# Optimization experiments

Hardware: AMD Instinct MI355X
Metric: run time of the kernel (lower is better)

Reference implementation:

```python
import jax, jax.numpy as jnp
import numpy as np

B, N, HIDDEN = 4, 2048, 512
N_HEADS, HEAD_DIM = 8, 64
N_CANCER = 32
SCALE = float(np.sqrt(HEAD_DIM))


def setup_inputs() -> dict:
    key = jax.random.key(0)
    ks = jax.random.split(key, 16)
    s = 0.02
    return {
        "x": jax.random.normal(ks[0], (B, N, HIDDEN), dtype=jnp.float32),
        "cancer_type": jax.random.randint(ks[1], (B,), 0, N_CANCER, dtype=jnp.int64),
        "attn_mask": jnp.zeros((B, N), dtype=bool),
        "wq": jax.random.normal(ks[2], (HIDDEN, HIDDEN), dtype=jnp.float32) * s,
        "bq": jnp.zeros((HIDDEN,), dtype=jnp.float32),
        "wk": jax.random.normal(ks[3], (HIDDEN, HIDDEN), dtype=jnp.float32) * s,
        "bk": jnp.zeros((HIDDEN,), dtype=jnp.float32),
        "wv": jax.random.normal(ks[4], (HIDDEN, HIDDEN), dtype=jnp.float32) * s,
        "bv": jnp.zeros((HIDDEN,), dtype=jnp.float32),
        "wo": jax.random.normal(ks[5], (HIDDEN, HIDDEN), dtype=jnp.float32) * s,
        "bo": jnp.zeros((HIDDEN,), dtype=jnp.float32),
        "bias_emb": jax.random.normal(ks[6], (N_CANCER, N_HEADS), dtype=jnp.float32) * s,
        "keymod_emb": jax.random.normal(ks[7], (N_CANCER, HIDDEN), dtype=jnp.float32) * s,
    }


def reference(x, cancer_type, attn_mask, wq, bq, wk, bk, wv, bv, wo, bo, bias_emb, keymod_emb):
    Bc, Nc, _ = x.shape
    # projections (torch Linear: x @ W.T + b), split heads -> (B, H, N, D)
    def split_heads(t):
        return t.reshape(Bc, Nc, N_HEADS, HEAD_DIM).transpose(0, 2, 1, 3)
    q = split_heads(x @ wq.T + bq)
    k = split_heads(x @ wk.T + bk)
    v = split_heads(x @ wv.T + bv)
    # cancer-conditioned key offset: (B, H, 1, D)
    ct_key = keymod_emb[cancer_type].reshape(Bc, 1, N_HEADS, HEAD_DIM).transpose(0, 2, 1, 3)
    k = k + ct_key
    # scores + per-head cancer bias
    attn = jnp.einsum("bhnd,bhmd->bhnm", q, k) / SCALE
    ct_bias = bias_emb[cancer_type]  # (B, H)
    attn = attn + ct_bias[:, :, None, None]
    attn = jnp.where(attn_mask[:, None, None, :], -jnp.inf, attn)
    attn = jax.nn.softmax(attn, axis=-1)
    # dropout is identity in eval mode
    out = jnp.einsum("bhnm,bhmd->bhnd", attn, v)
    out = out.transpose(0, 2, 1, 3).reshape(Bc, Nc, HIDDEN)
    return out @ wo.T + bo
```

## Files before the change

### kernel.cpp

```cpp
#include <hip/hip_runtime.h>

#define B_    4
#define N_    2048
#define HID   512
#define NH    8
#define HD    64
#define TOK   (B_ * N_)
#define LOG2E 1.4426950408889634f

typedef __attribute__((ext_vector_type(8))) short short8;
typedef __attribute__((ext_vector_type(4))) float f32x4;
typedef unsigned short u16;

static __device__ __forceinline__ u16 f2bf(float f) {
    unsigned int u = __builtin_bit_cast(unsigned int, f);
    u += 0x7FFFu + ((u >> 16) & 1u);
    return (u16)(u >> 16);
}
static __device__ __forceinline__ float bf2f(u16 v) {
    return __builtin_bit_cast(float, (unsigned)v << 16);
}
static __device__ __forceinline__ unsigned pktrunc(float a, float b) {
    return __builtin_amdgcn_perm(__builtin_bit_cast(unsigned, b),
                                 __builtin_bit_cast(unsigned, a), 0x07060302u);
}

static __device__ __forceinline__ void dma16(const void* g, void* l) {
    __builtin_amdgcn_global_load_lds(
        (const __attribute__((address_space(1))) unsigned int*)(unsigned long long)g,
        (__attribute__((address_space(3))) unsigned int*)(unsigned int)(unsigned long long)l,
        16, 0, 0);
}

__global__ __launch_bounds__(256) void cvt_all(
    const float* __restrict__ x,
    const float* __restrict__ w0, const float* __restrict__ w1,
    const float* __restrict__ w2, const float* __restrict__ w3,
    u16* __restrict__ xb,
    u16* __restrict__ d0, u16* __restrict__ d1,
    u16* __restrict__ d2, u16* __restrict__ d3)
{
    const int bid = blockIdx.x;
    const float* s;
    u16* d;
    int off;
    if (bid < 4096) { s = x; d = xb; off = bid; }
    else {
        const int t = (bid - 4096) >> 8;
        off = (bid - 4096) & 255;
        s = t == 0 ? w0 : t == 1 ? w1 : t == 2 ? w2 : w3;
        d = t == 0 ? d0 : t == 1 ? d1 : t == 2 ? d2 : d3;
    }
    const int i = off * 1024 + threadIdx.x * 4;
    const float4 v = *(const float4*)&s[i];
    ushort4 o;
    o.x = f2bf(v.x); o.y = f2bf(v.y); o.z = f2bf(v.z); o.w = f2bf(v.w);
    *(ushort4*)&d[i] = o;
}

__global__ __launch_bounds__(256) void gemm_qkv(
    const u16* __restrict__ xb,
    const u16* __restrict__ W0, const u16* __restrict__ W1, const u16* __restrict__ W2,
    const float* __restrict__ bias0, const float* __restrict__ bias1, const float* __restrict__ bias2,
    u16* __restrict__ Qg, u16* __restrict__ Kg, u16* __restrict__ Vtg)
{
    const int z = blockIdx.z;
    const u16*   Wz   = z == 0 ? W0 : z == 1 ? W1 : W2;
    const float* bias = z == 0 ? bias0 : z == 1 ? bias1 : bias2;

    const u16* Ap; const u16* Bp; int arow0, brow0;
    if (z < 2) { Ap = Wz; Bp = xb; arow0 = blockIdx.y * 128; brow0 = blockIdx.x * 128; }
    else       { Ap = xb; Bp = Wz; arow0 = blockIdx.x * 128; brow0 = blockIdx.y * 128; }

    __shared__ u16 ABs[2][2][128 * 32];

    const int tid  = threadIdx.x;
    const int w    = tid >> 6, lane = tid & 63;
    const int wr   = w >> 1, wc = w & 1;
    const int t16  = lane & 15, q4 = lane >> 4;

    const int dmr  = lane >> 2;
    const int dmc8 = (lane & 3) ^ ((lane >> 2) & 3) ^ ((lane >> 4) & 3);

    f32x4 acc[4][4];
    #pragma unroll
    for (int mt = 0; mt < 4; ++mt)
        #pragma unroll
        for (int nt = 0; nt < 4; ++nt)
            acc[mt][nt] = (f32x4){0.f, 0.f, 0.f, 0.f};

    #define QKV_DMA(p, k0)                                                      \
        _Pragma("unroll")                                                       \
        for (int i = 0; i < 2; ++i) {                                           \
            const int c = w * 2 + i;                                            \
            dma16(&Ap[(size_t)(arow0 + c * 16 + dmr) * HID + (k0) + dmc8 * 8],  \
                  &ABs[p][0][c * 512]);                                         \
            dma16(&Bp[(size_t)(brow0 + c * 16 + dmr) * HID + (k0) + dmc8 * 8],  \
                  &ABs[p][1][c * 512]);                                         \
        }

    const int swz = (t16 ^ (t16 >> 2)) & 3;

    auto qstep = [&](const int p) {
        short8 af[4], bf[4];
        #pragma unroll
        for (int mt = 0; mt < 4; ++mt)
            af[mt] = *(const short8*)&ABs[p][0][(wr * 64 + mt * 16 + t16) * 32 + (q4 ^ swz) * 8];
        #pragma unroll
        for (int nt = 0; nt < 4; ++nt)
            bf[nt] = *(const short8*)&ABs[p][1][(wc * 64 + nt * 16 + t16) * 32 + (q4 ^ swz) * 8];
        #pragma unroll
        for (int mt = 0; mt < 4; ++mt)
            #pragma unroll
            for (int nt = 0; nt < 4; ++nt)
                acc[mt][nt] = __builtin_amdgcn_mfma_f32_16x16x32_bf16(
                    af[mt], bf[nt], acc[mt][nt], 0, 0, 0);
    };

    QKV_DMA(0, 0)
    for (int it = 0; it < 16; it += 2) {
        __syncthreads();
        QKV_DMA(1, (it + 1) * 32)
        qstep(0);
        __syncthreads();
        if (it + 2 < 16) { QKV_DMA(0, (it + 2) * 32) }
        qstep(1);
    }

    if (z < 2) {
        const float qs = (z == 0) ? 0.125f * LOG2E : 1.0f;
        u16* Cg = (z == 0) ? Qg : Kg;
        u16 (*St)[72] = (u16(*)[72])&ABs[0][0][0];
        #pragma unroll
        for (int p = 0; p < 2; ++p) {
            __syncthreads();
            if (wr == p) {
                #pragma unroll
                for (int mt = 0; mt < 4; ++mt) {
                    const f32x4 bv = *(const f32x4*)&bias[arow0 + p * 64 + mt * 16 + q4 * 4];
                    #pragma unroll
                    for (int nt = 0; nt < 4; ++nt) {
                        const int np = wc * 64 + nt * 16 + t16;
                        uint2 pk;
                        pk.x = pktrunc((acc[mt][nt][0] + bv[0]) * qs,
                                       (acc[mt][nt][1] + bv[1]) * qs);
                        pk.y = pktrunc((acc[mt][nt][2] + bv[2]) * qs,
                                       (acc[mt][nt][3] + bv[3]) * qs);
                        *(uint2*)&St[np][mt * 16 + q4 * 4] = pk;
                    }
                }
            }
            __syncthreads();
            const int h = blockIdx.y * 2 + p;
            #pragma unroll
            for (int it = 0; it < 4; ++it) {
                const int task = tid + it * 256;
                const int np = task >> 3, ch = task & 7;
                const int nf = brow0 + np;
                const int b = nf >> 11, n = nf & (N_ - 1);
                *(short8*)&Cg[(((size_t)(b * NH + h)) * N_ + n) * HD + ch * 8] =
                    *(const short8*)&St[np][ch * 8];
            }
        }
    } else {
        u16 (*St)[72] = (u16(*)[72])&ABs[0][0][0];
        const int b = arow0 >> 11;
        #pragma unroll
        for (int p = 0; p < 2; ++p) {
            __syncthreads();
            if (wr == p) {
                #pragma unroll
                for (int nt = 0; nt < 4; ++nt) {
                    const int jp = wc * 64 + nt * 16 + t16;
                    const float bv = bias[brow0 + jp];
                    #pragma unroll
                    for (int mt = 0; mt < 4; ++mt) {
                        uint2 pk;
                        pk.x = pktrunc(acc[mt][nt][0] + bv, acc[mt][nt][1] + bv);
                        pk.y = pktrunc(acc[mt][nt][2] + bv, acc[mt][nt][3] + bv);
                        *(uint2*)&St[jp][mt * 16 + q4 * 4] = pk;
                    }
                }
            }
            __syncthreads();
            const int nb = (arow0 & (N_ - 1)) + p * 64;
            #pragma unroll
            for (int it = 0; it < 2; ++it) {
                const int task = tid + it * 256;
                const int jp = task >> 2, qc = task & 3;
                u16 v[16];
                #pragma unroll
                for (int e = 0; e < 16; ++e) {
                    const int np = qc * 16 + e;
                    const int n  = ((np & 3) << 4) | (np >> 2);
                    v[e] = St[jp][n];
                }
                const int j = brow0 + jp, h = j >> 6, d = j & 63;
                u16* dst = &Vtg[(((size_t)(b * NH + h)) * HD + d) * N_ + nb + qc * 16];
                *(short8*)(dst)     = *(const short8*)&v[0];
                *(short8*)(dst + 8) = *(const short8*)&v[8];
            }
        }
    }
}

__global__ __launch_bounds__(256) void flash_mfma(
    const u16* __restrict__ Qg, const u16* __restrict__ Kg,
    const u16* __restrict__ Vtg, const unsigned char* __restrict__ msk,
    u16* __restrict__ Op, float* __restrict__ Lp)
{
    __shared__ u16 KVs[2][2][64 * 64];
    __shared__ u16 Ps[4][32][72];
    __shared__ unsigned Mnd[16][32];

    const int tid = threadIdx.x;
    const int w = tid >> 6, lane = tid & 63;
    const int t16 = lane & 15, q4 = lane >> 4;
    const int bh = blockIdx.y, b = bh >> 3;
    const int z = blockIdx.z;
    const int kofs = z * (N_ / 2);
    const int qrow0 = blockIdx.x * 128;
    const int qbase = qrow0 + w * 32;

    const size_t hb = (size_t)bh * N_ * HD;
    const u16* Qh  = Qg + hb;
    const u16* Kh  = Kg + hb;
    const u16* Vth = Vtg + hb;
    const unsigned char* mrow = msk + b * N_;

    #pragma unroll
    for (int it = 0; it < 2; ++it) {
        const int e = tid + it * 256;
        const int kt = e >> 5, sl = e & 31;
        const int tt = sl >> 1, wd = sl & 1;
        const int k0 = kofs + kt * 64 + wd * 32 + tt;
        const unsigned lo = mrow[k0]      ? 0u : 0x0000FFFFu;
        const unsigned hi = mrow[k0 + 16] ? 0u : 0xFFFF0000u;
        Mnd[kt][sl] = lo | hi;
    }

    short8 qf[2][2];
    #pragma unroll
    for (int mt = 0; mt < 2; ++mt)
        #pragma unroll
        for (int kk = 0; kk < 2; ++kk)
            qf[mt][kk] = *(const short8*)
                &Qh[(size_t)(qbase + mt * 16 + t16) * HD + kk * 32 + q4 * 8];

    const short8 ones8 = {0x3F80, 0x3F80, 0x3F80, 0x3F80,
                          0x3F80, 0x3F80, 0x3F80, 0x3F80};

    f32x4 o[2][4], ls[2];
    #pragma unroll
    for (int mt = 0; mt < 2; ++mt) {
        #pragma unroll
        for (int nt = 0; nt < 4; ++nt) o[mt][nt] = (f32x4){0.f, 0.f, 0.f, 0.f};
        ls[mt] = (f32x4){0.f, 0.f, 0.f, 0.f};
    }

    const int dmr  = lane >> 3;
    const int dmc8 = (lane & 7) ^ ((lane >> 3) & 7);

    #define FLASH_DMA(p, kb)                                                    \
        _Pragma("unroll")                                                       \
        for (int i = 0; i < 2; ++i) {                                           \
            const int c = w * 2 + i;                                            \
            dma16(&Kh[(size_t)((kb) + c * 8 + dmr) * HD + dmc8 * 8],            \
                  &KVs[p][0][c * 512]);                                         \
            dma16(&Vth[(size_t)(c * 8 + dmr) * N_ + (kb) + dmc8 * 8],           \
                  &KVs[p][1][c * 512]);                                         \
        }

    const int swz7 = t16 & 7;

    auto fstep = [&](const int p, const int kt) {
        f32x4 s[2][4];
        #pragma unroll
        for (int mt = 0; mt < 2; ++mt)
            #pragma unroll
            for (int f = 0; f < 4; ++f)
                s[mt][f] = (f32x4){0.f, 0.f, 0.f, 0.f};
        #pragma unroll
        for (int f = 0; f < 4; ++f) {
            #pragma unroll
            for (int kk = 0; kk < 2; ++kk) {
                const short8 kf = *(const short8*)
                    &KVs[p][0][(f * 16 + t16) * 64 + ((kk * 4 + q4) ^ swz7) * 8];
                #pragma unroll
                for (int mt = 0; mt < 2; ++mt)
                    s[mt][f] = __builtin_amdgcn_mfma_f32_16x16x32_bf16(
                        qf[mt][kk], kf, s[mt][f], 0, 0, 0);
            }
        }

        const uint2 mnd = *(const uint2*)&Mnd[kt][t16 * 2];

        #pragma unroll
        for (int mt = 0; mt < 2; ++mt) {
            #pragma unroll
            for (int r = 0; r < 4; ++r) {
                const float e0 = __builtin_amdgcn_exp2f(s[mt][0][r]);
                const float e1 = __builtin_amdgcn_exp2f(s[mt][1][r]);
                const float e2 = __builtin_amdgcn_exp2f(s[mt][2][r]);
                const float e3 = __builtin_amdgcn_exp2f(s[mt][3][r]);
                uint2 pk;
                pk.x = pktrunc(e0, e1) & mnd.x;
                pk.y = pktrunc(e2, e3) & mnd.y;
                *(uint2*)&Ps[w][mt * 16 + q4 * 4 + r][t16 * 4] = pk;
            }
        }

        short8 pf[2][2];
        #pragma unroll
        for (int mt = 0; mt < 2; ++mt)
            #pragma unroll
            for (int kk = 0; kk < 2; ++kk)
                pf[mt][kk] = *(const short8*)&Ps[w][mt * 16 + t16][kk * 32 + q4 * 8];
        #pragma unroll
        for (int mt = 0; mt < 2; ++mt)
            #pragma unroll
            for (int kk = 0; kk < 2; ++kk)
                ls[mt] = __builtin_amdgcn_mfma_f32_16x16x32_bf16(
                    pf[mt][kk], ones8, ls[mt], 0, 0, 0);
        #pragma unroll
        for (int nt = 0; nt < 4; ++nt) {
            #pragma unroll
            for (int kk = 0; kk < 2; ++kk) {
                const short8 vf = *(const short8*)
                    &KVs[p][1][(nt * 16 + t16) * 64 + ((kk * 4 + q4) ^ swz7) * 8];
                #pragma unroll
                for (int mt = 0; mt < 2; ++mt)
                    o[mt][nt] = __builtin_amdgcn_mfma_f32_16x16x32_bf16(
                        pf[mt][kk], vf, o[mt][nt], 0, 0, 0);
            }
        }
    };

    FLASH_DMA(0, kofs)
    for (int kt = 0; kt < 16; kt += 2) {
        __syncthreads();
        FLASH_DMA(1, kofs + (kt + 1) * 64)
        fstep(0, kt);
        __syncthreads();
        if (kt + 2 < 16) { FLASH_DMA(0, kofs + (kt + 2) * 64) }
        fstep(1, kt + 1);
    }

    const size_t obase = (((size_t)z * 32 + bh)) * N_ * HD;
    #pragma unroll
    for (int mt = 0; mt < 2; ++mt) {
        #pragma unroll
        for (int r = 0; r < 4; ++r) {
            const int n = qbase + mt * 16 + q4 * 4 + r;
            if (t16 == 0) Lp[((size_t)z * 32 + bh) * N_ + n] = ls[mt][r];
            #pragma unroll
            for (int nt = 0; nt < 4; ++nt)
                Op[obase + (size_t)n * HD + nt * 16 + t16] = f2bf(o[mt][nt][r]);
        }
    }
}

__global__ __launch_bounds__(256) void gemm_o2(
    const u16* __restrict__ Op, const float* __restrict__ Lp,
    const u16* __restrict__ W, const float* __restrict__ bias,
    float* __restrict__ C)
{
    __shared__ u16 As[2][32][40];
    __shared__ u16 Bs[2][128 * 32];

    const int tid  = threadIdx.x;
    const int row0 = blockIdx.x * 32, col0 = blockIdx.y * 128;
    const int w    = tid >> 6, lane = tid & 63;
    const int wr   = w >> 1, wc = w & 1;
    const int t16  = lane & 15, q4 = lane >> 4;

    const int dmr  = lane >> 2;
    const int dmc8 = (lane & 3) ^ ((lane >> 2) & 3) ^ ((lane >> 4) & 3);

    f32x4 acc[4];
    #pragma unroll
    for (int nt = 0; nt < 4; ++nt) acc[nt] = (f32x4){0.f, 0.f, 0.f, 0.f};

    #define O2_DMA(p, k0)                                                       \
        _Pragma("unroll")                                                       \
        for (int i = 0; i < 2; ++i) {                                           \
            const int c = w * 2 + i;                                            \
            dma16(&W[(size_t)(col0 + c * 16 + dmr) * HID + (k0) + dmc8 * 8],    \
                  &Bs[p][c * 512]);                                             \
        }

    const int tr = tid >> 2, dcol = (tid & 3) * 8;
    const int itok = row0 + tr;
    const int ab = itok >> 11, an = itok & (N_ - 1);
    short8 a0, a1;
    float inv;
    const size_t OP_HALF = (size_t)32 * N_ * HD;

    auto aload = [&](const int t) {
        const int h = t >> 1, dk = (t & 1) * 32;
        const size_t li  = ((size_t)(ab * NH + h)) * N_ + an;
        const size_t off = li * HD + dk + dcol;
        a0 = *(const short8*)&Op[off];
        a1 = *(const short8*)&Op[off + OP_HALF];
        inv = 1.f / (Lp[li] + Lp[li + (size_t)32 * N_]);
    };

    const int swz = (t16 ^ (t16 >> 2)) & 3;

    auto ostep = [&](const int p, const int t) {
        if (tid < 128) {
            float v[8];
            #pragma unroll
            for (int i = 0; i < 8; ++i)
                v[i] = (bf2f((u16)a0[i]) + bf2f((u16)a1[i])) * inv;
            uint4 pk;
            pk.x = pktrunc(v[0], v[1]);
            pk.y = pktrunc(v[2], v[3]);
            pk.z = pktrunc(v[4], v[5]);
            pk.w = pktrunc(v[6], v[7]);
            *(uint4*)&As[p][tr][dcol] = pk;
        }
        __syncthreads();
        if (t + 1 < 16) {
            O2_DMA(p ^ 1, (t + 1) * 32)
            if (tid < 128) aload(t + 1);
        }
        const short8 af = *(const short8*)&As[p][wr * 16 + t16][q4 * 8];
        short8 bf[4];
        #pragma unroll
        for (int nt = 0; nt < 4; ++nt)
            bf[nt] = *(const short8*)&Bs[p][(wc * 64 + nt * 16 + t16) * 32 + (q4 ^ swz) * 8];
        #pragma unroll
        for (int nt = 0; nt < 4; ++nt)
            acc[nt] = __builtin_amdgcn_mfma_f32_16x16x32_bf16(af, bf[nt], acc[nt], 0, 0, 0);
    };

    O2_DMA(0, 0)
    if (tid < 128) aload(0);
    for (int t = 0; t < 16; t += 2) {
        ostep(0, t);
        ostep(1, t + 1);
    }

    #pragma unroll
    for (int nt = 0; nt < 4; ++nt) {
        const int j = col0 + wc * 64 + nt * 16 + t16;
        const float bv = bias[j];
        #pragma unroll
        for (int r = 0; r < 4; ++r) {
            const int i = row0 + wr * 16 + q4 * 4 + r;
            C[(size_t)i * HID + j] = acc[nt][r] + bv;
        }
    }
}

extern "C" void kernel_launch(void* const* d_in, const int* in_sizes, int n_in,
                              void* d_out, int out_size, void* d_ws, size_t ws_size,
                              hipStream_t stream) {
    const float* x  = (const float*)d_in[0];
    const unsigned char* mask = (const unsigned char*)d_in[2];
    const float* wq = (const float*)d_in[3];
    const float* bq = (const float*)d_in[4];
    const float* wk = (const float*)d_in[5];
    const float* bk = (const float*)d_in[6];
    const float* wv = (const float*)d_in[7];
    const float* bv = (const float*)d_in[8];
    const float* wo = (const float*)d_in[9];
    const float* bo = (const float*)d_in[10];

    char* ws = (char*)d_ws;
    u16* xb  = (u16*)(ws);
    u16* wqb = (u16*)(ws + (8u << 20));
    u16* wkb = (u16*)(ws + (8u << 20) + (512u << 10));
    u16* wvb = (u16*)(ws + (8u << 20) + (1024u << 10));
    u16* wob = (u16*)(ws + (8u << 20) + (1536u << 10));
    u16* Qg  = (u16*)(ws + (10u << 20));
    u16* Kg  = (u16*)(ws + (18u << 20));
    u16* Vtg = (u16*)(ws + (26u << 20));
    u16* Op  = (u16*)(ws + (34u << 20));
    float* Lp = (float*)(ws + (50u << 20));

    cvt_all<<<5120, 256, 0, stream>>>(x, wq, wk, wv, wo, xb, wqb, wkb, wvb, wob);

    gemm_qkv<<<dim3(TOK / 128, HID / 128, 3), 256, 0, stream>>>(
        xb, wqb, wkb, wvb, bq, bk, bv, Qg, Kg, Vtg);

    flash_mfma<<<dim3(N_ / 128, B_ * NH, 2), 256, 0, stream>>>(
        Qg, Kg, Vtg, mask, Op, Lp);

    gemm_o2<<<dim3(TOK / 32, HID / 128), 256, 0, stream>>>(
        Op, Lp, wob, bo, (float*)d_out);
}
```

Measured before the change: 178.8 us.

## Double per-wave query rows in flash kernel and row tile in output GEMM

```diff
diff --git a/kernel.cpp b/kernel.cpp
--- a/kernel.cpp
+++ b/kernel.cpp
@@ -204,13 +204,13 @@
     }
 }
 
-__global__ __launch_bounds__(256) void flash_mfma(
+__global__ __launch_bounds__(256, 2) void flash_mfma(
     const u16* __restrict__ Qg, const u16* __restrict__ Kg,
     const u16* __restrict__ Vtg, const unsigned char* __restrict__ msk,
     u16* __restrict__ Op, float* __restrict__ Lp)
 {
     __shared__ u16 KVs[2][2][64 * 64];
-    __shared__ u16 Ps[4][32][72];
+    __shared__ u16 Ps[4][64][72];
     __shared__ unsigned Mnd[16][32];
 
     const int tid = threadIdx.x;
@@ -219,8 +219,8 @@
     const int bh = blockIdx.y, b = bh >> 3;
     const int z = blockIdx.z;
     const int kofs = z * (N_ / 2);
-    const int qrow0 = blockIdx.x * 128;
-    const int qbase = qrow0 + w * 32;
+    const int qrow0 = blockIdx.x * 256;
+    const int qbase = qrow0 + w * 64;
 
     const size_t hb = (size_t)bh * N_ * HD;
     const u16* Qh  = Qg + hb;
@@ -239,9 +239,9 @@
         Mnd[kt][sl] = lo | hi;
     }
 
-    short8 qf[2][2];
-    #pragma unroll
-    for (int mt = 0; mt < 2; ++mt)
+    short8 qf[4][2];
+    #pragma unroll
+    for (int mt = 0; mt < 4; ++mt)
         #pragma unroll
         for (int kk = 0; kk < 2; ++kk)
             qf[mt][kk] = *(const short8*)
@@ -250,9 +250,9 @@
     const short8 ones8 = {0x3F80, 0x3F80, 0x3F80, 0x3F80,
                           0x3F80, 0x3F80, 0x3F80, 0x3F80};
 
-    f32x4 o[2][4], ls[2];
-    #pragma unroll
-    for (int mt = 0; mt < 2; ++mt) {
+    f32x4 o[4][4], ls[4];
+    #pragma unroll
+    for (int mt = 0; mt < 4; ++mt) {
         #pragma unroll
         for (int nt = 0; nt < 4; ++nt) o[mt][nt] = (f32x4){0.f, 0.f, 0.f, 0.f};
         ls[mt] = (f32x4){0.f, 0.f, 0.f, 0.f};
@@ -274,9 +274,9 @@
     const int swz7 = t16 & 7;
 
     auto fstep = [&](const int p, const int kt) {
-        f32x4 s[2][4];
-        #pragma unroll
-        for (int mt = 0; mt < 2; ++mt)
+        f32x4 s[4][4];
+        #pragma unroll
+        for (int mt = 0; mt < 4; ++mt)
             #pragma unroll
             for (int f = 0; f < 4; ++f)
                 s[mt][f] = (f32x4){0.f, 0.f, 0.f, 0.f};
@@ -287,7 +287,7 @@
                 const short8 kf = *(const short8*)
                     &KVs[p][0][(f * 16 + t16) * 64 + ((kk * 4 + q4) ^ swz7) * 8];
                 #pragma unroll
-                for (int mt = 0; mt < 2; ++mt)
+                for (int mt = 0; mt < 4; ++mt)
                     s[mt][f] = __builtin_amdgcn_mfma_f32_16x16x32_bf16(
                         qf[mt][kk], kf, s[mt][f], 0, 0, 0);
             }
@@ -296,7 +296,7 @@
         const uint2 mnd = *(const uint2*)&Mnd[kt][t16 * 2];
 
         #pragma unroll
-        for (int mt = 0; mt < 2; ++mt) {
+        for (int mt = 0; mt < 4; ++mt) {
             #pragma unroll
             for (int r = 0; r < 4; ++r) {
                 const float e0 = __builtin_amdgcn_exp2f(s[mt][0][r]);
@@ -310,14 +310,14 @@
             }
         }
 
-        short8 pf[2][2];
-        #pragma unroll
-        for (int mt = 0; mt < 2; ++mt)
+        short8 pf[4][2];
+        #pragma unroll
+        for (int mt = 0; mt < 4; ++mt)
             #pragma unroll
             for (int kk = 0; kk < 2; ++kk)
                 pf[mt][kk] = *(const short8*)&Ps[w][mt * 16 + t16][kk * 32 + q4 * 8];
         #pragma unroll
-        for (int mt = 0; mt < 2; ++mt)
+        for (int mt = 0; mt < 4; ++mt)
             #pragma unroll
             for (int kk = 0; kk < 2; ++kk)
                 ls[mt] = __builtin_amdgcn_mfma_f32_16x16x32_bf16(
@@ -329,7 +329,7 @@
                 const short8 vf = *(const short8*)
                     &KVs[p][1][(nt * 16 + t16) * 64 + ((kk * 4 + q4) ^ swz7) * 8];
                 #pragma unroll
-                for (int mt = 0; mt < 2; ++mt)
+                for (int mt = 0; mt < 4; ++mt)
                     o[mt][nt] = __builtin_amdgcn_mfma_f32_16x16x32_bf16(
                         pf[mt][kk], vf, o[mt][nt], 0, 0, 0);
             }
@@ -348,7 +348,7 @@
 
     const size_t obase = (((size_t)z * 32 + bh)) * N_ * HD;
     #pragma unroll
-    for (int mt = 0; mt < 2; ++mt) {
+    for (int mt = 0; mt < 4; ++mt) {
         #pragma unroll
         for (int r = 0; r < 4; ++r) {
             const int n = qbase + mt * 16 + q4 * 4 + r;
@@ -365,11 +365,11 @@
     const u16* __restrict__ W, const float* __restrict__ bias,
     float* __restrict__ C)
 {
-    __shared__ u16 As[2][32][40];
+    __shared__ u16 As[2][64][40];
     __shared__ u16 Bs[2][128 * 32];
 
     const int tid  = threadIdx.x;
-    const int row0 = blockIdx.x * 32, col0 = blockIdx.y * 128;
+    const int row0 = blockIdx.x * 64, col0 = blockIdx.y * 128;
     const int w    = tid >> 6, lane = tid & 63;
     const int wr   = w >> 1, wc = w & 1;
     const int t16  = lane & 15, q4 = lane >> 4;
@@ -377,9 +377,11 @@
     const int dmr  = lane >> 2;
     const int dmc8 = (lane & 3) ^ ((lane >> 2) & 3) ^ ((lane >> 4) & 3);
 
-    f32x4 acc[4];
-    #pragma unroll
-    for (int nt = 0; nt < 4; ++nt) acc[nt] = (f32x4){0.f, 0.f, 0.f, 0.f};
+    f32x4 acc[2][4];
+    #pragma unroll
+    for (int mt = 0; mt < 2; ++mt)
+        #pragma unroll
+        for (int nt = 0; nt < 4; ++nt) acc[mt][nt] = (f32x4){0.f, 0.f, 0.f, 0.f};
 
     #define O2_DMA(p, k0)                                                       \
         _Pragma("unroll")                                                       \
@@ -408,7 +410,7 @@
     const int swz = (t16 ^ (t16 >> 2)) & 3;
 
     auto ostep = [&](const int p, const int t) {
-        if (tid < 128) {
+        {
             float v[8];
             #pragma unroll
             for (int i = 0; i < 8; ++i)
@@ -423,20 +425,25 @@
         __syncthreads();
         if (t + 1 < 16) {
             O2_DMA(p ^ 1, (t + 1) * 32)
-            if (tid < 128) aload(t + 1);
-        }
-        const short8 af = *(const short8*)&As[p][wr * 16 + t16][q4 * 8];
-        short8 bf[4];
+            aload(t + 1);
+        }
+        short8 af[2], bf[4];
+        #pragma unroll
+        for (int mt = 0; mt < 2; ++mt)
+            af[mt] = *(const short8*)&As[p][wr * 32 + mt * 16 + t16][q4 * 8];
         #pragma unroll
         for (int nt = 0; nt < 4; ++nt)
             bf[nt] = *(const short8*)&Bs[p][(wc * 64 + nt * 16 + t16) * 32 + (q4 ^ swz) * 8];
         #pragma unroll
-        for (int nt = 0; nt < 4; ++nt)
-            acc[nt] = __builtin_amdgcn_mfma_f32_16x16x32_bf16(af, bf[nt], acc[nt], 0, 0, 0);
+        for (int mt = 0; mt < 2; ++mt)
+            #pragma unroll
+            for (int nt = 0; nt < 4; ++nt)
+                acc[mt][nt] = __builtin_amdgcn_mfma_f32_16x16x32_bf16(
+                    af[mt], bf[nt], acc[mt][nt], 0, 0, 0);
     };
 
     O2_DMA(0, 0)
-    if (tid < 128) aload(0);
+    aload(0);
     for (int t = 0; t < 16; t += 2) {
         ostep(0, t);
         ostep(1, t + 1);
@@ -447,10 +454,12 @@
         const int j = col0 + wc * 64 + nt * 16 + t16;
         const float bv = bias[j];
         #pragma unroll
-        for (int r = 0; r < 4; ++r) {
-            const int i = row0 + wr * 16 + q4 * 4 + r;
-            C[(size_t)i * HID + j] = acc[nt][r] + bv;
-        }
+        for (int mt = 0; mt < 2; ++mt)
+            #pragma unroll
+            for (int r = 0; r < 4; ++r) {
+                const int i = row0 + wr * 32 + mt * 16 + q4 * 4 + r;
+                C[(size_t)i * HID + j] = acc[mt][nt][r] + bv;
+            }
     }
 }
 
@@ -485,9 +494,9 @@
     gemm_qkv<<<dim3(TOK / 128, HID / 128, 3), 256, 0, stream>>>(
         xb, wqb, wkb, wvb, bq, bk, bv, Qg, Kg, Vtg);
 
-    flash_mfma<<<dim3(N_ / 128, B_ * NH, 2), 256, 0, stream>>>(
+    flash_mfma<<<dim3(N_ / 256, B_ * NH, 2), 256, 0, stream>>>(
         Qg, Kg, Vtg, mask, Op, Lp);
 
-    gemm_o2<<<dim3(TOK / 32, HID / 128), 256, 0, stream>>>(
+    gemm_o2<<<dim3(TOK / 64, HID / 128), 256, 0, stream>>>(
         Op, Lp, wob, bo, (float*)d_out);
 }
```

Result: faster. 169.5 us (-5.2%).
